# Kernel tuning notes

Measured on AMD Instinct MI355X. Metric: run time of the kernel, lower is better.

Reference implementation:

```python
import jax, jax.numpy as jnp
import numpy as np

EPS = 1e-05


def setup_inputs() -> dict:
    key = jax.random.key(0)
    ks = jax.random.split(key, 4)
    B, N, D, H, E = 16, 8192, 128, 64, 64
    x = jax.random.normal(ks[0], (B, N, D), dtype=jnp.float32)
    ln_w = jnp.ones((D,), jnp.float32)
    ln_b = jnp.zeros((D,), jnp.float32)
    Wl = jax.random.normal(ks[1], (D, H), dtype=jnp.float32) / np.sqrt(D)
    bl = jnp.zeros((H,), jnp.float32)
    Wr = jax.random.normal(ks[2], (D, H), dtype=jnp.float32) / np.sqrt(D)
    br = jnp.zeros((H,), jnp.float32)
    Wo = jax.random.normal(ks[3], (H, E), dtype=jnp.float32) / np.sqrt(H)
    bo = jnp.zeros((E,), jnp.float32)
    return {"x": x, "ln_w": ln_w, "ln_b": ln_b, "Wl": Wl, "bl": bl,
            "Wr": Wr, "br": br, "Wo": Wo, "bo": bo}


def _layernorm(x, w, b):
    mu = jnp.mean(x, axis=-1, keepdims=True)
    var = jnp.mean(jnp.square(x - mu), axis=-1, keepdims=True)
    return (x - mu) * jax.lax.rsqrt(var + EPS) * w + b


def reference(x, ln_w, ln_b, Wl, bl, Wr, br, Wo, bo):
    # x: [B, N, D]
    xn = _layernorm(x, ln_w, ln_b)
    left = xn @ Wl + bl    # [B, N, H]
    right = xn @ Wr + br   # [B, N, H]
    # Original: einsum('b i d, b j d -> b i j d').mean(dim=1).
    # Identical math without the O(N^2) tensor: mean over i factors out of
    # the product since left[b,i,d]*right[b,j,d] is separable in i.
    outer = left.mean(axis=1)[:, None, :] * right  # [B, N, H]
    return outer @ Wo + bo  # [B, N, E]
```

## Files before the change

### kernel.cpp

```cpp
#include <hip/hip_runtime.h>
#include <math.h>

#define B_  16
#define N_  8192
#define D_  128
#define H_  64
#define E_  64
#define EPSLN 1e-5f

typedef __attribute__((ext_vector_type(8))) short short8;
typedef __attribute__((ext_vector_type(4))) float f32x4;

#define WSB_PART 0
#define WSB_WRT  262144
#define WSB_U    278528
#define WSB_Q    278784
#define WSB_W2T  279040
#define WSB_C2   410112
#define WSB_Z    1048576

static __device__ __forceinline__ unsigned short f2bf(float f) {
    union { float f; unsigned u; } c; c.f = f;
    unsigned u = c.u;
    return (unsigned short)((u + 0x7FFFu + ((u >> 16) & 1u)) >> 16);
}
static __device__ __forceinline__ float bf2f(short v) {
    union { unsigned u; float f; } c;
    c.u = ((unsigned)(unsigned short)v) << 16;
    return c.f;
}

__global__ __launch_bounds__(256) void k_prep(const float* __restrict__ ln_w,
                                              const float* __restrict__ ln_b,
                                              const float* __restrict__ Wr,
                                              unsigned short* __restrict__ Wrt,
                                              float* __restrict__ ug,
                                              float* __restrict__ qg) {
    __shared__ float ru[4][H_], rq[4][H_];
    int t = threadIdx.x;
    int h = t & 63, dq = t >> 6;
    float u = 0.f, q = 0.f;
    for (int i = 0; i < 32; ++i) {
        int d = dq * 32 + i;
        float wr = Wr[d * H_ + h];
        float lw = ln_w[d];
        u += lw * wr;
        q += ln_b[d] * wr;
        Wrt[h * D_ + d] = f2bf(lw * wr);
    }
    ru[dq][h] = u; rq[dq][h] = q;
    __syncthreads();
    if (t < H_) {
        ug[t] = ru[0][t] + ru[1][t] + ru[2][t] + ru[3][t];
        qg[t] = rq[0][t] + rq[1][t] + rq[2][t] + rq[3][t];
    }
}

__global__ __launch_bounds__(256, 2) void k_pass1(const float* __restrict__ x,
                                                  const unsigned short* __restrict__ Wrt,
                                                  const float* __restrict__ ug,
                                                  const float* __restrict__ qg,
                                                  float* __restrict__ partials,
                                                  unsigned short* __restrict__ Zg) {
    __shared__ short xs[256 * 128];
    __shared__ float mul[256], rsl[256];
    __shared__ float redc[4][128];
    __shared__ float ush[H_], qsh[H_];

    int b = blockIdx.y, bx = blockIdx.x, t = threadIdx.x;
    int rowbase = bx * 256;

    if (t < H_) { ush[t] = ug[t]; qsh[t] = qg[t]; }

    {
        const float4* xrow = (const float4*)(x + (size_t)(b * N_ + rowbase + t) * D_);
        float s = 0.f, s2 = 0.f;
        int sw = t & 15;
#pragma unroll
        for (int g = 0; g < 16; ++g) {
            float4 va = xrow[2 * g], vb = xrow[2 * g + 1];
            s  += (va.x + va.y) + (va.z + va.w) + (vb.x + vb.y) + (vb.z + vb.w);
            s2 += (va.x * va.x + va.y * va.y) + (va.z * va.z + va.w * va.w)
                + (vb.x * vb.x + vb.y * vb.y) + (vb.z * vb.z + vb.w * vb.w);
            short8 sv;
            sv[0] = (short)f2bf(va.x); sv[1] = (short)f2bf(va.y);
            sv[2] = (short)f2bf(va.z); sv[3] = (short)f2bf(va.w);
            sv[4] = (short)f2bf(vb.x); sv[5] = (short)f2bf(vb.y);
            sv[6] = (short)f2bf(vb.z); sv[7] = (short)f2bf(vb.w);
            *(short8*)&xs[t * 128 + ((g ^ sw) * 8)] = sv;
        }
        float mu  = s * (1.f / D_);
        float var = s2 * (1.f / D_) - mu * mu;
        mul[t] = mu;
        rsl[t] = rsqrtf(var + EPSLN);
    }
    __syncthreads();

    {
        int cp = (t & 63) * 2, q = t >> 6;
        int g = cp >> 3, jo = cp & 7;
        float a0 = 0.f, a1 = 0.f;
#pragma unroll 8
        for (int i = 0; i < 64; ++i) {
            int r = q * 64 + i;
            short2 v = *(const short2*)&xs[r * 128 + ((g ^ (r & 15)) * 8) + jo];
            float w = rsl[r], m = mul[r];
            a0 += w * (bf2f(v.x) - m);
            a1 += w * (bf2f(v.y) - m);
        }
        redc[q][cp] = a0;
        redc[q][cp + 1] = a1;
    }
    __syncthreads();
    if (t < 128) {
        float s = redc[0][t] + redc[1][t] + redc[2][t] + redc[3][t];
        partials[(size_t)(b * 32 + bx) * D_ + t] = s;
    }

    int wv = t >> 6, lane = t & 63;
    int m16 = lane & 15, quad = lane >> 4;

    f32x4 acc[4][4];
#pragma unroll
    for (int i = 0; i < 4; ++i)
#pragma unroll
        for (int j = 0; j < 4; ++j) acc[i][j] = (f32x4){0.f, 0.f, 0.f, 0.f};

#pragma unroll
    for (int kc = 0; kc < 4; ++kc) {
        short8 af[4], bf[4];
#pragma unroll
        for (int mt = 0; mt < 4; ++mt) {
            int row = wv * 64 + mt * 16 + m16;
            int g = kc * 4 + quad;
            af[mt] = *(const short8*)&xs[row * 128 + ((g ^ m16) * 8)];
        }
#pragma unroll
        for (int nt = 0; nt < 4; ++nt) {
            bf[nt] = *(const short8*)(Wrt + (size_t)(nt * 16 + m16) * D_ + kc * 32 + quad * 8);
        }
#pragma unroll
        for (int mt = 0; mt < 4; ++mt)
#pragma unroll
            for (int nt = 0; nt < 4; ++nt)
                acc[mt][nt] = __builtin_amdgcn_mfma_f32_16x16x32_bf16(
                    af[mt], bf[nt], acc[mt][nt], 0, 0, 0);
    }

    size_t zbase = (size_t)(b * N_ + rowbase) * H_;
#pragma unroll
    for (int mt = 0; mt < 4; ++mt) {
        int rb = wv * 64 + mt * 16 + quad * 4;
        float mu0 = mul[rb + 0], rs0 = rsl[rb + 0];
        float mu1 = mul[rb + 1], rs1 = rsl[rb + 1];
        float mu2 = mul[rb + 2], rs2 = rsl[rb + 2];
        float mu3 = mul[rb + 3], rs3 = rsl[rb + 3];
#pragma unroll
        for (int nt = 0; nt < 4; ++nt) {
            int col = nt * 16 + m16;
            float uc = ush[col], qc = qsh[col];
            unsigned short* zp = Zg + zbase + (size_t)rb * H_ + col;
            zp[0 * H_] = f2bf(rs0 * (acc[mt][nt][0] - mu0 * uc) + qc);
            zp[1 * H_] = f2bf(rs1 * (acc[mt][nt][1] - mu1 * uc) + qc);
            zp[2 * H_] = f2bf(rs2 * (acc[mt][nt][2] - mu2 * uc) + qc);
            zp[3 * H_] = f2bf(rs3 * (acc[mt][nt][3] - mu3 * uc) + qc);
        }
    }
}

__global__ __launch_bounds__(256) void k_combine2(const float* __restrict__ partials,
                                                  const float* __restrict__ ln_w,
                                                  const float* __restrict__ ln_b,
                                                  const float* __restrict__ Wl,
                                                  const float* __restrict__ bl,
                                                  const float* __restrict__ br,
                                                  const float* __restrict__ Wo,
                                                  const float* __restrict__ bo,
                                                  unsigned short* __restrict__ W2t,
                                                  float* __restrict__ C2g) {
    __shared__ float cm[D_], mlh[H_];
    __shared__ float redC[4][E_];
    int b = blockIdx.x, t = threadIdx.x;

    if (t < D_) {
        float s = 0.f;
#pragma unroll 8
        for (int k = 0; k < 32; ++k)
            s += partials[(size_t)(b * 32 + k) * D_ + t];
        cm[t] = ln_w[t] * s * (1.f / N_) + ln_b[t];
    }
    __syncthreads();
    if (t < H_) {
        float a = bl[t];
        for (int d = 0; d < D_; ++d) a += cm[d] * Wl[d * H_ + t];
        mlh[t] = a;
    }
    __syncthreads();

    int e = t & 63, hq = t >> 6;
    float cpart = 0.f;
    size_t wb = (size_t)b * E_ * H_;
    for (int i = 0; i < 16; ++i) {
        int h = hq * 16 + i;
        float wo = Wo[h * E_ + e];
        float w2 = mlh[h] * wo;
        cpart += w2 * br[h];
        W2t[wb + (size_t)e * H_ + h] = f2bf(w2);
    }
    redC[hq][e] = cpart;
    __syncthreads();
    if (t < E_)
        C2g[b * E_ + t] = redC[0][t] + redC[1][t] + redC[2][t] + redC[3][t] + bo[t];
}

__global__ __launch_bounds__(256) void k_pass2(const unsigned short* __restrict__ Zg,
                                               const unsigned short* __restrict__ W2t,
                                               const float* __restrict__ C2g,
                                               float* __restrict__ out) {
    __shared__ float C2l[E_];
    int b = blockIdx.y, bx = blockIdx.x, t = threadIdx.x;
    int rowbase = bx * 256;
    if (t < E_) C2l[t] = C2g[b * E_ + t];
    __syncthreads();

    int wv = t >> 6, lane = t & 63;
    int m16 = lane & 15, quad = lane >> 4;

    f32x4 acc[4][4];
#pragma unroll
    for (int i = 0; i < 4; ++i)
#pragma unroll
        for (int j = 0; j < 4; ++j) acc[i][j] = (f32x4){0.f, 0.f, 0.f, 0.f};

    size_t zbase = (size_t)(b * N_ + rowbase) * H_;
    const unsigned short* Wb = W2t + (size_t)b * E_ * H_;

#pragma unroll
    for (int kc = 0; kc < 2; ++kc) {
        short8 af[4], bf[4];
#pragma unroll
        for (int mt = 0; mt < 4; ++mt) {
            int row = wv * 64 + mt * 16 + m16;
            af[mt] = *(const short8*)(Zg + zbase + (size_t)row * H_ + kc * 32 + quad * 8);
        }
#pragma unroll
        for (int nt = 0; nt < 4; ++nt) {
            bf[nt] = *(const short8*)(Wb + (size_t)(nt * 16 + m16) * H_ + kc * 32 + quad * 8);
        }
#pragma unroll
        for (int mt = 0; mt < 4; ++mt)
#pragma unroll
            for (int nt = 0; nt < 4; ++nt)
                acc[mt][nt] = __builtin_amdgcn_mfma_f32_16x16x32_bf16(
                    af[mt], bf[nt], acc[mt][nt], 0, 0, 0);
    }

    size_t outbase = (size_t)(b * N_ + rowbase) * E_;
#pragma unroll
    for (int mt = 0; mt < 4; ++mt) {
        int rb = wv * 64 + mt * 16 + quad * 4;
#pragma unroll
        for (int nt = 0; nt < 4; ++nt) {
            int col = nt * 16 + m16;
            float Cc = C2l[col];
            float* o = out + outbase + (size_t)rb * E_ + col;
            o[0 * E_] = acc[mt][nt][0] + Cc;
            o[1 * E_] = acc[mt][nt][1] + Cc;
            o[2 * E_] = acc[mt][nt][2] + Cc;
            o[3 * E_] = acc[mt][nt][3] + Cc;
        }
    }
}

extern "C" void kernel_launch(void* const* d_in, const int* in_sizes, int n_in,
                              void* d_out, int out_size, void* d_ws, size_t ws_size,
                              hipStream_t stream) {
    const float* x    = (const float*)d_in[0];
    const float* ln_w = (const float*)d_in[1];
    const float* ln_b = (const float*)d_in[2];
    const float* Wl   = (const float*)d_in[3];
    const float* bl   = (const float*)d_in[4];
    const float* Wr   = (const float*)d_in[5];
    const float* br   = (const float*)d_in[6];
    const float* Wo   = (const float*)d_in[7];
    const float* bo   = (const float*)d_in[8];
    float* out = (float*)d_out;
    char* ws   = (char*)d_ws;

    float*          partials = (float*)(ws + WSB_PART);
    unsigned short* Wrt      = (unsigned short*)(ws + WSB_WRT);
    float*          ug       = (float*)(ws + WSB_U);
    float*          qg       = (float*)(ws + WSB_Q);
    unsigned short* W2t      = (unsigned short*)(ws + WSB_W2T);
    float*          C2g      = (float*)(ws + WSB_C2);
    unsigned short* Zg       = (unsigned short*)(ws + WSB_Z);

    k_prep<<<1, 256, 0, stream>>>(ln_w, ln_b, Wr, Wrt, ug, qg);
    k_pass1<<<dim3(32, B_), 256, 0, stream>>>(x, Wrt, ug, qg, partials, Zg);
    k_combine2<<<B_, 256, 0, stream>>>(partials, ln_w, ln_b, Wl, bl, br, Wo,
                                       bo, W2t, C2g);
    k_pass2<<<dim3(32, B_), 256, 0, stream>>>(Zg, W2t, C2g, out);
}
```

Baseline: 148.8 us.

## Fuse combine into pass1 via last-block atomic counter and coalesce x loads

Removes the separate k_combine2 launch. The last block per batch, found with an atomic counter reset in k_prep, now computes the column means, W2t and C2 at the end of pass1. The x load is also restructured so 16 consecutive threads share one row, which gives coalesced float4 loads, a shuffle reduction for the layernorm stats, and packed bf16 conversion. The cost is extra atomics and fences, plus a serial tail in one block per batch.

```diff
diff --git a/kernel.cpp b/kernel.cpp
--- a/kernel.cpp
+++ b/kernel.cpp
@@ -1,4 +1,5 @@
 #include <hip/hip_runtime.h>
+#include <hip/hip_bf16.h>
 #include <math.h>
 
 #define B_  16
@@ -12,11 +13,12 @@
 typedef __attribute__((ext_vector_type(4))) float f32x4;
 
 #define WSB_PART 0
-#define WSB_WRT  262144
-#define WSB_U    278528
-#define WSB_Q    278784
-#define WSB_W2T  279040
-#define WSB_C2   410112
+#define WSB_CTR  262144
+#define WSB_WRT  262208
+#define WSB_U    278592
+#define WSB_Q    278848
+#define WSB_W2T  279104
+#define WSB_C2   410176
 #define WSB_Z    1048576
 
 static __device__ __forceinline__ unsigned short f2bf(float f) {
@@ -35,9 +37,11 @@
                                               const float* __restrict__ Wr,
                                               unsigned short* __restrict__ Wrt,
                                               float* __restrict__ ug,
-                                              float* __restrict__ qg) {
+                                              float* __restrict__ qg,
+                                              int* __restrict__ ctr) {
     __shared__ float ru[4][H_], rq[4][H_];
     int t = threadIdx.x;
+    if (t < 16) ctr[t] = 0;
     int h = t & 63, dq = t >> 6;
     float u = 0.f, q = 0.f;
     for (int i = 0; i < 32; ++i) {
@@ -60,12 +64,23 @@
                                                   const unsigned short* __restrict__ Wrt,
                                                   const float* __restrict__ ug,
                                                   const float* __restrict__ qg,
+                                                  const float* __restrict__ ln_w,
+                                                  const float* __restrict__ ln_b,
+                                                  const float* __restrict__ Wl,
+                                                  const float* __restrict__ bl,
+                                                  const float* __restrict__ br,
+                                                  const float* __restrict__ Wo,
+                                                  const float* __restrict__ bo,
                                                   float* __restrict__ partials,
+                                                  int* __restrict__ ctr,
+                                                  unsigned short* __restrict__ W2t,
+                                                  float* __restrict__ C2g,
                                                   unsigned short* __restrict__ Zg) {
     __shared__ short xs[256 * 128];
     __shared__ float mul[256], rsl[256];
     __shared__ float redc[4][128];
     __shared__ float ush[H_], qsh[H_];
+    __shared__ int   isl;
 
     int b = blockIdx.y, bx = blockIdx.x, t = threadIdx.x;
     int rowbase = bx * 256;
@@ -73,26 +88,34 @@
     if (t < H_) { ush[t] = ug[t]; qsh[t] = qg[t]; }
 
     {
-        const float4* xrow = (const float4*)(x + (size_t)(b * N_ + rowbase + t) * D_);
-        float s = 0.f, s2 = 0.f;
-        int sw = t & 15;
-#pragma unroll
-        for (int g = 0; g < 16; ++g) {
-            float4 va = xrow[2 * g], vb = xrow[2 * g + 1];
-            s  += (va.x + va.y) + (va.z + va.w) + (vb.x + vb.y) + (vb.z + vb.w);
-            s2 += (va.x * va.x + va.y * va.y) + (va.z * va.z + va.w * va.w)
-                + (vb.x * vb.x + vb.y * vb.y) + (vb.z * vb.z + vb.w * vb.w);
-            short8 sv;
-            sv[0] = (short)f2bf(va.x); sv[1] = (short)f2bf(va.y);
-            sv[2] = (short)f2bf(va.z); sv[3] = (short)f2bf(va.w);
-            sv[4] = (short)f2bf(vb.x); sv[5] = (short)f2bf(vb.y);
-            sv[6] = (short)f2bf(vb.z); sv[7] = (short)f2bf(vb.w);
-            *(short8*)&xs[t * 128 + ((g ^ sw) * 8)] = sv;
-        }
-        float mu  = s * (1.f / D_);
-        float var = s2 * (1.f / D_) - mu * mu;
-        mul[t] = mu;
-        rsl[t] = rsqrtf(var + EPSLN);
+        size_t tb4 = (size_t)(b * N_ + rowbase) * 32;
+        const float4* x4 = (const float4*)x;
+#pragma unroll
+        for (int k = 0; k < 16; ++k) {
+            int idx = t + 256 * k;
+            int row = idx >> 4, g = idx & 15;
+            float4 va = x4[tb4 + 2 * idx];
+            float4 vb = x4[tb4 + 2 * idx + 1];
+            float s  = (va.x + va.y) + (va.z + va.w) + (vb.x + vb.y) + (vb.z + vb.w);
+            float s2 = (va.x * va.x + va.y * va.y) + (va.z * va.z + va.w * va.w)
+                     + (vb.x * vb.x + vb.y * vb.y) + (vb.z * vb.z + vb.w * vb.w);
+            s  += __shfl_xor(s, 1, 16);  s2 += __shfl_xor(s2, 1, 16);
+            s  += __shfl_xor(s, 2, 16);  s2 += __shfl_xor(s2, 2, 16);
+            s  += __shfl_xor(s, 4, 16);  s2 += __shfl_xor(s2, 4, 16);
+            s  += __shfl_xor(s, 8, 16);  s2 += __shfl_xor(s2, 8, 16);
+            union { short8 s8; __hip_bfloat162 h2[4]; } u;
+            u.h2[0] = __float22bfloat162_rn(make_float2(va.x, va.y));
+            u.h2[1] = __float22bfloat162_rn(make_float2(va.z, va.w));
+            u.h2[2] = __float22bfloat162_rn(make_float2(vb.x, vb.y));
+            u.h2[3] = __float22bfloat162_rn(make_float2(vb.z, vb.w));
+            *(short8*)&xs[row * 128 + ((g ^ (row & 15)) * 8)] = u.s8;
+            if ((t & 15) == 0) {
+                float mu  = s * (1.f / D_);
+                float var = s2 * (1.f / D_) - mu * mu;
+                mul[row] = mu;
+                rsl[row] = rsqrtf(var + EPSLN);
+            }
+        }
     }
     __syncthreads();
 
@@ -116,6 +139,12 @@
         float s = redc[0][t] + redc[1][t] + redc[2][t] + redc[3][t];
         partials[(size_t)(b * 32 + bx) * D_ + t] = s;
     }
+    __syncthreads();
+    if (t == 0) {
+        __threadfence();
+        int old = atomicAdd(&ctr[b], 1);
+        isl = (old == 31);
+    }
 
     int wv = t >> 6, lane = t & 63;
     int m16 = lane & 15, quad = lane >> 4;
@@ -166,21 +195,14 @@
             zp[3 * H_] = f2bf(rs3 * (acc[mt][nt][3] - mu3 * uc) + qc);
         }
     }
-}
-
-__global__ __launch_bounds__(256) void k_combine2(const float* __restrict__ partials,
-                                                  const float* __restrict__ ln_w,
-                                                  const float* __restrict__ ln_b,
-                                                  const float* __restrict__ Wl,
-                                                  const float* __restrict__ bl,
-                                                  const float* __restrict__ br,
-                                                  const float* __restrict__ Wo,
-                                                  const float* __restrict__ bo,
-                                                  unsigned short* __restrict__ W2t,
-                                                  float* __restrict__ C2g) {
-    __shared__ float cm[D_], mlh[H_];
-    __shared__ float redC[4][E_];
-    int b = blockIdx.x, t = threadIdx.x;
+
+    __syncthreads();
+    if (!isl) return;
+    __threadfence();
+
+    float* cm   = &redc[0][0];
+    float* mlh  = &redc[1][0];
+    float* redC = &redc[2][0];
 
     if (t < D_) {
         float s = 0.f;
@@ -207,10 +229,11 @@
         cpart += w2 * br[h];
         W2t[wb + (size_t)e * H_ + h] = f2bf(w2);
     }
-    redC[hq][e] = cpart;
+    redC[hq * 64 + e] = cpart;
     __syncthreads();
     if (t < E_)
-        C2g[b * E_ + t] = redC[0][t] + redC[1][t] + redC[2][t] + redC[3][t] + bo[t];
+        C2g[b * E_ + t] = redC[0 * 64 + t] + redC[1 * 64 + t]
+                        + redC[2 * 64 + t] + redC[3 * 64 + t] + bo[t];
 }
 
 __global__ __launch_bounds__(256) void k_pass2(const unsigned short* __restrict__ Zg,
@@ -288,6 +311,7 @@
     char* ws   = (char*)d_ws;
 
     float*          partials = (float*)(ws + WSB_PART);
+    int*            ctr      = (int*)(ws + WSB_CTR);
     unsigned short* Wrt      = (unsigned short*)(ws + WSB_WRT);
     float*          ug       = (float*)(ws + WSB_U);
     float*          qg       = (float*)(ws + WSB_Q);
@@ -295,9 +319,9 @@
     float*          C2g      = (float*)(ws + WSB_C2);
     unsigned short* Zg       = (unsigned short*)(ws + WSB_Z);
 
-    k_prep<<<1, 256, 0, stream>>>(ln_w, ln_b, Wr, Wrt, ug, qg);
-    k_pass1<<<dim3(32, B_), 256, 0, stream>>>(x, Wrt, ug, qg, partials, Zg);
-    k_combine2<<<B_, 256, 0, stream>>>(partials, ln_w, ln_b, Wl, bl, br, Wo,
-                                       bo, W2t, C2g);
+    k_prep<<<1, 256, 0, stream>>>(ln_w, ln_b, Wr, Wrt, ug, qg, ctr);
+    k_pass1<<<dim3(32, B_), 256, 0, stream>>>(x, Wrt, ug, qg, ln_w, ln_b, Wl,
+                                              bl, br, Wo, bo, partials, ctr,
+                                              W2t, C2g, Zg);
     k_pass2<<<dim3(32, B_), 256, 0, stream>>>(Zg, W2t, C2g, out);
 }
```

Result: slower. 182.4 us (+22.6%).
